# Performance work log

Hardware: AMD Instinct MI355X
Metric: run time of the kernel (lower is better)

Reference implementation:

```python
import math
import jax, jax.numpy as jnp
import numpy as np

B, L, D = 16, 2048, 64  # batch, seq len (m == n, self-attention), head dim
C = 30                   # ProbSparse sampling factor c


def setup_inputs() -> dict:
    key = jax.random.key(0)
    kq, kk, kv = jax.random.split(key, 3)
    Q = jax.random.normal(kq, (B, L, D), dtype=jnp.float32)
    K = jax.random.normal(kk, (B, L, D), dtype=jnp.float32)
    V = jax.random.normal(kv, (B, L, D), dtype=jnp.float32)
    return {"Q": Q, "K": K, "V": V, "seed": 0}


def reference(Q, K, V, seed):
    b, m, d = Q.shape
    n = K.shape[1]
    u = int(C * math.log(m))              # number of active queries
    U = min(int(m * math.log(n)), n)      # number of sampled keys (clamped to n)
    inv_sqrt_d = 1.0 / math.sqrt(d)

    rngs = jax.random.split(jax.random.key(seed), b)

    def _each_sample(Qb, Kb, Vb, r):
        # random sample of U key rows without replacement
        idx = jax.random.choice(r, n, shape=(U,), replace=False)
        Kbar = Kb[idx]                                # [U, d]
        Sbar = jnp.matmul(Qb, Kbar.T)                 # [m, U]
        M = jnp.max(Sbar, axis=1) - jnp.mean(Sbar, axis=1)  # sparsity measure [m]
        _, I = jax.lax.top_k(M, u)                    # active query indices [u]
        Qbar = Qb[I]                                  # [u, d]
        A = jax.nn.softmax(jnp.matmul(Qbar, Kb.T) * inv_sqrt_d, axis=-1)  # [u, n]
        S1 = jnp.matmul(A, Vb)                        # [u, d]
        # literal source: fill with mean(V, axis=1, keepdims=True) -> (n,1) broadcast (m==n)
        S = jnp.broadcast_to(jnp.mean(Vb, axis=1, keepdims=True), (m, d))
        return S.at[I].set(S1)

    return jax.vmap(_each_sample)(Q, K, V, rngs)
```

## Files before the change

### kernel.cpp

```cpp
#include <hip/hip_runtime.h>

#define NB 16
#define NN 2048
#define DH 64
#define NSEL 228
#define KS 8
#define CHUNK (NN / KS)
#define RS 8

__global__ __launch_bounds__(256, 2) void rowstat_kernel(const float* __restrict__ Q,
                                                         const float* __restrict__ K,
                                                         float* __restrict__ Mmax,
                                                         float* __restrict__ Msum) {
  __shared__ float Qt[32][128];
  __shared__ float Kt[32][128];
  const int b = blockIdx.y;
  const int cz = blockIdx.z;
  const int qbase = blockIdx.x * 128;
  const int tid = threadIdx.x;
  const int r = tid & 127;
  const int h16 = (tid >> 7) * 16;
  const int ty = tid >> 4;
  const int tx = tid & 15;
  const float* Qb = Q + ((size_t)b * NN + qbase) * DH;
  const float* Kb = K + ((size_t)b * NN + cz * (NN / RS)) * DH;

  float rmax[8], rsum[8];
  #pragma unroll
  for (int a = 0; a < 8; ++a) { rmax[a] = -3.0e38f; rsum[a] = 0.f; }

  for (int kt = 0; kt < NN / RS / 128; ++kt) {
    float acc[8][8];
    #pragma unroll
    for (int a = 0; a < 8; ++a)
      #pragma unroll
      for (int c = 0; c < 8; ++c) acc[a][c] = 0.f;

    #pragma unroll
    for (int half = 0; half < 2; ++half) {
      const int d0 = half * 32;
      __syncthreads();
      {
        const float* qs = Qb + r * DH + d0 + h16;
        const float* ks = Kb + ((size_t)(kt * 128 + r)) * DH + d0 + h16;
        #pragma unroll
        for (int f = 0; f < 4; ++f) {
          float4 v = *reinterpret_cast<const float4*>(qs + f * 4);
          Qt[h16 + f * 4 + 0][r] = v.x;
          Qt[h16 + f * 4 + 1][r] = v.y;
          Qt[h16 + f * 4 + 2][r] = v.z;
          Qt[h16 + f * 4 + 3][r] = v.w;
          float4 w = *reinterpret_cast<const float4*>(ks + f * 4);
          Kt[h16 + f * 4 + 0][r] = w.x;
          Kt[h16 + f * 4 + 1][r] = w.y;
          Kt[h16 + f * 4 + 2][r] = w.z;
          Kt[h16 + f * 4 + 3][r] = w.w;
        }
      }
      __syncthreads();

      #pragma unroll 2
      for (int d = 0; d < 32; ++d) {
        float qv[8], kv[8];
        *reinterpret_cast<float4*>(qv) =
            *reinterpret_cast<const float4*>(&Qt[d][ty * 4]);
        *reinterpret_cast<float4*>(qv + 4) =
            *reinterpret_cast<const float4*>(&Qt[d][64 + ty * 4]);
        *reinterpret_cast<float4*>(kv) =
            *reinterpret_cast<const float4*>(&Kt[d][tx * 4]);
        *reinterpret_cast<float4*>(kv + 4) =
            *reinterpret_cast<const float4*>(&Kt[d][64 + tx * 4]);
        #pragma unroll
        for (int a = 0; a < 8; ++a)
          #pragma unroll
          for (int c = 0; c < 8; ++c) acc[a][c] = fmaf(qv[a], kv[c], acc[a][c]);
      }
    }

    #pragma unroll
    for (int a = 0; a < 8; ++a)
      #pragma unroll
      for (int c = 0; c < 8; ++c) {
        rmax[a] = fmaxf(rmax[a], acc[a][c]);
        rsum[a] += acc[a][c];
      }
  }

  #pragma unroll
  for (int off = 1; off < 16; off <<= 1) {
    #pragma unroll
    for (int a = 0; a < 8; ++a) {
      rmax[a] = fmaxf(rmax[a], __shfl_xor(rmax[a], off));
      rsum[a] += __shfl_xor(rsum[a], off);
    }
  }
  if (tx == 0) {
    #pragma unroll
    for (int a = 0; a < 8; ++a) {
      const int qlocal = (a >> 2) * 64 + ty * 4 + (a & 3);
      const size_t idx = ((size_t)cz * NB + b) * NN + qbase + qlocal;
      Mmax[idx] = rmax[a];
      Msum[idx] = rsum[a];
    }
  }
}

__global__ __launch_bounds__(256) void select_kernel(const float* __restrict__ Mmax,
                                                     const float* __restrict__ Msum,
                                                     int* __restrict__ Isel) {
  __shared__ int red[4];
  const int b = blockIdx.x;
  const int tid = threadIdx.x;
  const int lane = tid & 63;
  const int wid = tid >> 6;
  const int base = tid * 8;

  unsigned int kreg[8];
  #pragma unroll
  for (int f = 0; f < 8; ++f) {
    const int i = base + f;
    float mv = -3.0e38f, sv = 0.f;
    #pragma unroll
    for (int cz = 0; cz < RS; ++cz) {
      const size_t idx = ((size_t)cz * NB + b) * NN + i;
      mv = fmaxf(mv, Mmax[idx]);
      sv += Msum[idx];
    }
    const float M = mv - sv * (1.0f / NN);
    const unsigned int uu = __float_as_uint(M);
    kreg[f] = (uu & 0x80000000u) ? ~uu : (uu | 0x80000000u);
  }

  unsigned int v = 0u;
  for (int bit = 31; bit >= 0; --bit) {
    const unsigned int cand = v | (1u << bit);
    int c = 0;
    #pragma unroll
    for (int f = 0; f < 8; ++f) c += (kreg[f] >= cand) ? 1 : 0;
    #pragma unroll
    for (int off = 1; off < 64; off <<= 1) c += __shfl_xor(c, off);
    if (lane == 0) red[wid] = c;
    __syncthreads();
    const int total = red[0] + red[1] + red[2] + red[3];
    if (total >= NSEL) v = cand;
    __syncthreads();
  }

  int flg[8];
  int cnt = 0;
  #pragma unroll
  for (int f = 0; f < 8; ++f) { flg[f] = (kreg[f] > v) ? 1 : 0; cnt += flg[f]; }
  int scan = cnt;
  #pragma unroll
  for (int off = 1; off < 64; off <<= 1) {
    const int n = __shfl_up(scan, off);
    if (lane >= off) scan += n;
  }
  if (lane == 63) red[wid] = scan;
  __syncthreads();
  int wbase = 0;
  for (int w = 0; w < wid; ++w) wbase += red[w];
  const int cg = red[0] + red[1] + red[2] + red[3];
  int pos = wbase + scan - cnt;
  #pragma unroll
  for (int f = 0; f < 8; ++f)
    if (flg[f]) { Isel[b * NSEL + pos] = base + f; ++pos; }
  __syncthreads();

  const int need = NSEL - cg;
  cnt = 0;
  #pragma unroll
  for (int f = 0; f < 8; ++f) { flg[f] = (kreg[f] == v) ? 1 : 0; cnt += flg[f]; }
  scan = cnt;
  #pragma unroll
  for (int off = 1; off < 64; off <<= 1) {
    const int n = __shfl_up(scan, off);
    if (lane >= off) scan += n;
  }
  if (lane == 63) red[wid] = scan;
  __syncthreads();
  wbase = 0;
  for (int w = 0; w < wid; ++w) wbase += red[w];
  pos = wbase + scan - cnt;
  #pragma unroll
  for (int f = 0; f < 8; ++f)
    if (flg[f]) {
      if (pos < need) Isel[b * NSEL + cg + pos] = base + f;
      ++pos;
    }
}

__global__ __launch_bounds__(256) void fill_kernel(const float* __restrict__ V,
                                                   float* __restrict__ out) {
  const size_t row = (size_t)blockIdx.x * 4 + (threadIdx.x >> 6);
  const int lane = threadIdx.x & 63;
  float x = V[row * DH + lane];
  #pragma unroll
  for (int off = 1; off < 64; off <<= 1) x += __shfl_xor(x, off);
  out[row * DH + lane] = x * (1.0f / DH);
}

__global__ __launch_bounds__(256) void attn_part_kernel(const float* __restrict__ Q,
                                                        const float* __restrict__ K,
                                                        const float* __restrict__ V,
                                                        const int* __restrict__ Isel,
                                                        float* __restrict__ Pm,
                                                        float* __restrict__ Pl,
                                                        float* __restrict__ Po) {
  __shared__ float Qt[64][32];
  __shared__ float Kt[64][64];
  __shared__ float Vs[64][64];
  __shared__ float Pt[64][36];
  const int b = blockIdx.z;
  const int kc = blockIdx.y;
  const int g = blockIdx.x;
  const int tid = threadIdx.x;
  const int wq = tid >> 5;
  const int kx = tid & 31;

  if (tid < 128) {
    const int rr = tid >> 2;
    const int dblk = (tid & 3) * 16;
    const int lq = g * 32 + rr;
    const int qidx = (lq < NSEL) ? Isel[b * NSEL + lq] : 0;
    const float* qs = Q + ((size_t)b * NN + qidx) * DH + dblk;
    #pragma unroll
    for (int f = 0; f < 4; ++f) {
      float4 v = *reinterpret_cast<const float4*>(qs + f * 4);
      Qt[dblk + f * 4 + 0][rr] = v.x;
      Qt[dblk + f * 4 + 1][rr] = v.y;
      Qt[dblk + f * 4 + 2][rr] = v.z;
      Qt[dblk + f * 4 + 3][rr] = v.w;
    }
  }

  const float* Kb = K + ((size_t)b * NN + kc * CHUNK) * DH;
  const float* Vb = V + ((size_t)b * NN + kc * CHUNK) * DH;

  float m[4], lp[4], o[4][2];
  #pragma unroll
  for (int a = 0; a < 4; ++a) {
    m[a] = -3.0e38f; lp[a] = 0.f; o[a][0] = 0.f; o[a][1] = 0.f;
  }

  for (int st = 0; st < CHUNK / 64; ++st) {
    __syncthreads();
    {
      const int rr = tid & 63;
      const int dblk = (tid >> 6) * 16;
      const float* ks = Kb + ((size_t)(st * 64 + rr)) * DH + dblk;
      #pragma unroll
      for (int f = 0; f < 4; ++f) {
        float4 v = *reinterpret_cast<const float4*>(ks + f * 4);
        Kt[dblk + f * 4 + 0][rr] = v.x;
        Kt[dblk + f * 4 + 1][rr] = v.y;
        Kt[dblk + f * 4 + 2][rr] = v.z;
        Kt[dblk + f * 4 + 3][rr] = v.w;
      }
      const float* vsrc = Vb + (size_t)st * 64 * DH;
      float* vdst = &Vs[0][0];
      #pragma unroll
      for (int it = 0; it < 4; ++it) {
        const int fo = (it * 256 + tid) * 4;
        *reinterpret_cast<float4*>(vdst + fo) =
            *reinterpret_cast<const float4*>(vsrc + fo);
      }
    }
    __syncthreads();

    float sc[4][2];
    #pragma unroll
    for (int a = 0; a < 4; ++a) { sc[a][0] = 0.f; sc[a][1] = 0.f; }
    #pragma unroll 4
    for (int d = 0; d < 64; ++d) {
      float qv[4];
      *reinterpret_cast<float4*>(qv) =
          *reinterpret_cast<const float4*>(&Qt[d][wq * 4]);
      const float2 kv = *reinterpret_cast<const float2*>(&Kt[d][kx * 2]);
      #pragma unroll
      for (int a = 0; a < 4; ++a) {
        sc[a][0] = fmaf(qv[a], kv.x, sc[a][0]);
        sc[a][1] = fmaf(qv[a], kv.y, sc[a][1]);
      }
    }
    #pragma unroll
    for (int a = 0; a < 4; ++a) { sc[a][0] *= 0.125f; sc[a][1] *= 0.125f; }

    float tm[4];
    #pragma unroll
    for (int a = 0; a < 4; ++a) tm[a] = fmaxf(sc[a][0], sc[a][1]);
    #pragma unroll
    for (int off = 1; off < 32; off <<= 1) {
      #pragma unroll
      for (int a = 0; a < 4; ++a) tm[a] = fmaxf(tm[a], __shfl_xor(tm[a], off));
    }

    float w0[4], w1[4];
    #pragma unroll
    for (int a = 0; a < 4; ++a) {
      const float mn = fmaxf(m[a], tm[a]);
      const float scale = __expf(m[a] - mn);
      m[a] = mn;
      lp[a] *= scale;
      o[a][0] *= scale;
      o[a][1] *= scale;
      w0[a] = __expf(sc[a][0] - mn);
      w1[a] = __expf(sc[a][1] - mn);
      lp[a] += w0[a] + w1[a];
    }
    *reinterpret_cast<float4*>(&Pt[kx * 2][wq * 4]) =
        make_float4(w0[0], w0[1], w0[2], w0[3]);
    *reinterpret_cast<float4*>(&Pt[kx * 2 + 1][wq * 4]) =
        make_float4(w1[0], w1[1], w1[2], w1[3]);
    __syncthreads();

    #pragma unroll 4
    for (int k = 0; k < 64; ++k) {
      float pv[4];
      *reinterpret_cast<float4*>(pv) =
          *reinterpret_cast<const float4*>(&Pt[k][wq * 4]);
      const float2 vv = *reinterpret_cast<const float2*>(&Vs[k][kx * 2]);
      #pragma unroll
      for (int a = 0; a < 4; ++a) {
        o[a][0] = fmaf(pv[a], vv.x, o[a][0]);
        o[a][1] = fmaf(pv[a], vv.y, o[a][1]);
      }
    }
  }

  #pragma unroll
  for (int off = 1; off < 32; off <<= 1) {
    #pragma unroll
    for (int a = 0; a < 4; ++a) lp[a] += __shfl_xor(lp[a], off);
  }

  #pragma unroll
  for (int a = 0; a < 4; ++a) {
    const int lq = g * 32 + wq * 4 + a;
    if (lq < NSEL) {
      const size_t row = ((size_t)b * NSEL + lq) * KS + kc;
      if (kx == 0) { Pm[row] = m[a]; Pl[row] = lp[a]; }
      *reinterpret_cast<float2*>(Po + row * 64 + kx * 2) =
          make_float2(o[a][0], o[a][1]);
    }
  }
}

__global__ __launch_bounds__(256) void combine_kernel(const int* __restrict__ Isel,
                                                      const float* __restrict__ Pm,
                                                      const float* __restrict__ Pl,
                                                      const float* __restrict__ Po,
                                                      float* __restrict__ out) {
  const int r = blockIdx.x * 4 + (threadIdx.x >> 6);
  if (r >= NB * NSEL) return;
  const int lane = threadIdx.x & 63;
  const int b = r / NSEL;
  const int qidx = Isel[r];
  const size_t base = (size_t)r * KS;

  float pm[KS];
  float gm = -3.0e38f;
  #pragma unroll
  for (int c = 0; c < KS; ++c) { pm[c] = Pm[base + c]; gm = fmaxf(gm, pm[c]); }
  float L = 0.f, od = 0.f;
  #pragma unroll
  for (int c = 0; c < KS; ++c) {
    const float e = __expf(pm[c] - gm);
    L += Pl[base + c] * e;
    od += Po[(base + c) * 64 + lane] * e;
  }
  out[((size_t)b * NN + qidx) * DH + lane] = od / L;
}

extern "C" void kernel_launch(void* const* d_in, const int* in_sizes, int n_in,
                              void* d_out, int out_size, void* d_ws, size_t ws_size,
                              hipStream_t stream) {
  const float* Q = (const float*)d_in[0];
  const float* K = (const float*)d_in[1];
  const float* V = (const float*)d_in[2];
  float* out = (float*)d_out;

  float* Mmax = (float*)d_ws;
  float* Msum = Mmax + (size_t)RS * NB * NN;
  int* Isel = (int*)(Msum + (size_t)RS * NB * NN);
  float* Pm = (float*)(Isel + NB * NSEL);
  float* Pl = Pm + (size_t)NB * NSEL * KS;
  float* Po = Pl + (size_t)NB * NSEL * KS;

  rowstat_kernel<<<dim3(NN / 128, NB, RS), 256, 0, stream>>>(Q, K, Mmax, Msum);
  select_kernel<<<dim3(NB), 256, 0, stream>>>(Mmax, Msum, Isel);
  fill_kernel<<<dim3(NB * NN / 4), 256, 0, stream>>>(V, out);
  attn_part_kernel<<<dim3(8, KS, NB), 256, 0, stream>>>(Q, K, V, Isel, Pm, Pl, Po);
  combine_kernel<<<dim3((NB * NSEL + 3) / 4), 256, 0, stream>>>(Isel, Pm, Pl, Po, out);
}
```

Before: 254.4 us.

## Compute row max via split-bf16 MFMA and row mean via key column sums

Replaces the fp32 FMA row-statistics GEMM with a bf16 hi/lo split MFMA kernel (three products) and drops the per-row sum. Each row mean is now computed algebraically as Q·colsum(K)/N from a small column-sum kernel. Rows whose sparsity score falls within an epsilon band of the top-k threshold get an exact fp32 max recomputation before the final selection. This trades the full fp32 GEMM for tensor-core work plus conversion kernels, and relies on the epsilon band being wide enough to keep the selection exact.

```diff
diff --git a/kernel.cpp b/kernel.cpp
--- a/kernel.cpp
+++ b/kernel.cpp
@@ -6,131 +6,151 @@
 #define NSEL 228
 #define KS 8
 #define CHUNK (NN / KS)
-#define RS 8
-
-__global__ __launch_bounds__(256, 2) void rowstat_kernel(const float* __restrict__ Q,
-                                                         const float* __restrict__ K,
-                                                         float* __restrict__ Mmax,
-                                                         float* __restrict__ Msum) {
-  __shared__ float Qt[32][128];
-  __shared__ float Kt[32][128];
-  const int b = blockIdx.y;
-  const int cz = blockIdx.z;
+#define RS 4
+#define EPSBAND 2.0e-3f
+
+using s16x8 = __attribute__((ext_vector_type(8))) short;
+using f32x16 = __attribute__((ext_vector_type(16))) float;
+
+static __device__ __forceinline__ unsigned short f2bf(float x) {
+  unsigned int u = __float_as_uint(x);
+  u += 0x7fffu + ((u >> 16) & 1u);
+  return (unsigned short)(u >> 16);
+}
+static __device__ __forceinline__ float bf2f(unsigned short h) {
+  return __uint_as_float(((unsigned int)h) << 16);
+}
+static __device__ __forceinline__ unsigned int enc(float f) {
+  unsigned int u = __float_as_uint(f);
+  return (u & 0x80000000u) ? ~u : (u | 0x80000000u);
+}
+static __device__ __forceinline__ float dec(unsigned int k) {
+  return (k & 0x80000000u) ? __uint_as_float(k & 0x7fffffffu)
+                           : __uint_as_float(~k);
+}
+
+__global__ __launch_bounds__(256) void convk_kernel(const float* __restrict__ K,
+                                                    unsigned short* __restrict__ Khi,
+                                                    unsigned short* __restrict__ Klo) {
+  const size_t e = ((size_t)blockIdx.x * 256 + threadIdx.x) * 8;
+  float4 a = *(const float4*)(K + e);
+  float4 b = *(const float4*)(K + e + 4);
+  float v[8] = {a.x, a.y, a.z, a.w, b.x, b.y, b.z, b.w};
+  union { unsigned short u[8]; s16x8 s; } H, L;
+  #pragma unroll
+  for (int j = 0; j < 8; ++j) {
+    unsigned short h = f2bf(v[j]);
+    H.u[j] = h;
+    L.u[j] = f2bf(v[j] - bf2f(h));
+  }
+  *(s16x8*)(Khi + e) = H.s;
+  *(s16x8*)(Klo + e) = L.s;
+}
+
+__global__ __launch_bounds__(256) void kcolsum_kernel(const float* __restrict__ K,
+                                                      float* __restrict__ Kpart) {
+  __shared__ float part[4][64];
+  const int b = blockIdx.y, ch = blockIdx.x;
+  const int d = threadIdx.x & 63, g = threadIdx.x >> 6;
+  const float* Kb = K + ((size_t)b * NN + ch * 128) * DH;
+  float s = 0.f;
+  for (int r = g; r < 128; r += 4) s += Kb[r * DH + d];
+  part[g][d] = s;
+  __syncthreads();
+  if (threadIdx.x < 64)
+    Kpart[((size_t)b * 16 + ch) * 64 + threadIdx.x] =
+        part[0][threadIdx.x] + part[1][threadIdx.x] +
+        part[2][threadIdx.x] + part[3][threadIdx.x];
+}
+
+__global__ __launch_bounds__(256, 4) void rowstat_mfma(const float* __restrict__ Q,
+                                                       const unsigned short* __restrict__ Khi,
+                                                       const unsigned short* __restrict__ Klo,
+                                                       float* __restrict__ Mmax) {
+  __shared__ __align__(16) unsigned short KHs[128 * 64];
+  __shared__ __align__(16) unsigned short KLs[128 * 64];
+  const int b = blockIdx.y, cz = blockIdx.z;
   const int qbase = blockIdx.x * 128;
   const int tid = threadIdx.x;
-  const int r = tid & 127;
-  const int h16 = (tid >> 7) * 16;
-  const int ty = tid >> 4;
-  const int tx = tid & 15;
-  const float* Qb = Q + ((size_t)b * NN + qbase) * DH;
-  const float* Kb = K + ((size_t)b * NN + cz * (NN / RS)) * DH;
-
-  float rmax[8], rsum[8];
-  #pragma unroll
-  for (int a = 0; a < 8; ++a) { rmax[a] = -3.0e38f; rsum[a] = 0.f; }
-
-  for (int kt = 0; kt < NN / RS / 128; ++kt) {
-    float acc[8][8];
-    #pragma unroll
-    for (int a = 0; a < 8; ++a)
-      #pragma unroll
-      for (int c = 0; c < 8; ++c) acc[a][c] = 0.f;
-
-    #pragma unroll
-    for (int half = 0; half < 2; ++half) {
-      const int d0 = half * 32;
-      __syncthreads();
-      {
-        const float* qs = Qb + r * DH + d0 + h16;
-        const float* ks = Kb + ((size_t)(kt * 128 + r)) * DH + d0 + h16;
-        #pragma unroll
-        for (int f = 0; f < 4; ++f) {
-          float4 v = *reinterpret_cast<const float4*>(qs + f * 4);
-          Qt[h16 + f * 4 + 0][r] = v.x;
-          Qt[h16 + f * 4 + 1][r] = v.y;
-          Qt[h16 + f * 4 + 2][r] = v.z;
-          Qt[h16 + f * 4 + 3][r] = v.w;
-          float4 w = *reinterpret_cast<const float4*>(ks + f * 4);
-          Kt[h16 + f * 4 + 0][r] = w.x;
-          Kt[h16 + f * 4 + 1][r] = w.y;
-          Kt[h16 + f * 4 + 2][r] = w.z;
-          Kt[h16 + f * 4 + 3][r] = w.w;
-        }
-      }
-      __syncthreads();
-
-      #pragma unroll 2
-      for (int d = 0; d < 32; ++d) {
-        float qv[8], kv[8];
-        *reinterpret_cast<float4*>(qv) =
-            *reinterpret_cast<const float4*>(&Qt[d][ty * 4]);
-        *reinterpret_cast<float4*>(qv + 4) =
-            *reinterpret_cast<const float4*>(&Qt[d][64 + ty * 4]);
-        *reinterpret_cast<float4*>(kv) =
-            *reinterpret_cast<const float4*>(&Kt[d][tx * 4]);
-        *reinterpret_cast<float4*>(kv + 4) =
-            *reinterpret_cast<const float4*>(&Kt[d][64 + tx * 4]);
-        #pragma unroll
-        for (int a = 0; a < 8; ++a)
-          #pragma unroll
-          for (int c = 0; c < 8; ++c) acc[a][c] = fmaf(qv[a], kv[c], acc[a][c]);
-      }
-    }
-
-    #pragma unroll
-    for (int a = 0; a < 8; ++a)
-      #pragma unroll
-      for (int c = 0; c < 8; ++c) {
-        rmax[a] = fmaxf(rmax[a], acc[a][c]);
-        rsum[a] += acc[a][c];
-      }
-  }
-
-  #pragma unroll
-  for (int off = 1; off < 16; off <<= 1) {
-    #pragma unroll
-    for (int a = 0; a < 8; ++a) {
-      rmax[a] = fmaxf(rmax[a], __shfl_xor(rmax[a], off));
-      rsum[a] += __shfl_xor(rsum[a], off);
-    }
-  }
-  if (tx == 0) {
-    #pragma unroll
-    for (int a = 0; a < 8; ++a) {
-      const int qlocal = (a >> 2) * 64 + ty * 4 + (a & 3);
-      const size_t idx = ((size_t)cz * NB + b) * NN + qbase + qlocal;
-      Mmax[idx] = rmax[a];
-      Msum[idx] = rsum[a];
-    }
-  }
-}
-
-__global__ __launch_bounds__(256) void select_kernel(const float* __restrict__ Mmax,
-                                                     const float* __restrict__ Msum,
-                                                     int* __restrict__ Isel) {
-  __shared__ int red[4];
-  const int b = blockIdx.x;
-  const int tid = threadIdx.x;
-  const int lane = tid & 63;
-  const int wid = tid >> 6;
-  const int base = tid * 8;
-
-  unsigned int kreg[8];
-  #pragma unroll
-  for (int f = 0; f < 8; ++f) {
-    const int i = base + f;
-    float mv = -3.0e38f, sv = 0.f;
-    #pragma unroll
-    for (int cz = 0; cz < RS; ++cz) {
-      const size_t idx = ((size_t)cz * NB + b) * NN + i;
-      mv = fmaxf(mv, Mmax[idx]);
-      sv += Msum[idx];
-    }
-    const float M = mv - sv * (1.0f / NN);
-    const unsigned int uu = __float_as_uint(M);
-    kreg[f] = (uu & 0x80000000u) ? ~uu : (uu | 0x80000000u);
-  }
-
+  const int w = tid >> 6, lane = tid & 63;
+  const int l31 = lane & 31, hi5 = lane >> 5;
+
+  s16x8 qh[4], ql[4];
+  {
+    const float* qrow = Q + ((size_t)b * NN + qbase + w * 32 + l31) * DH;
+    #pragma unroll
+    for (int ks = 0; ks < 4; ++ks) {
+      const int d0 = ks * 16 + hi5 * 8;
+      float4 x = *(const float4*)(qrow + d0);
+      float4 y = *(const float4*)(qrow + d0 + 4);
+      float v[8] = {x.x, x.y, x.z, x.w, y.x, y.y, y.z, y.w};
+      union { unsigned short u[8]; s16x8 s; } H, L;
+      #pragma unroll
+      for (int j = 0; j < 8; ++j) {
+        unsigned short h = f2bf(v[j]);
+        H.u[j] = h;
+        L.u[j] = f2bf(v[j] - bf2f(h));
+      }
+      qh[ks] = H.s;
+      ql[ks] = L.s;
+    }
+  }
+
+  const size_t kbase = ((size_t)b * NN + cz * (NN / RS)) * DH;
+  f32x16 vmax;
+  #pragma unroll
+  for (int i = 0; i < 16; ++i) vmax[i] = -3.0e38f;
+
+  const int sr = tid >> 1;
+  const int sh = tid & 1;
+
+  for (int stage = 0; stage < NN / RS / 128; ++stage) {
+    __syncthreads();
+    {
+      const size_t g = kbase + (size_t)(stage * 128 + sr) * DH + sh * 32;
+      const unsigned short* gh = Khi + g;
+      const unsigned short* gl = Klo + g;
+      #pragma unroll
+      for (int c = 0; c < 4; ++c) {
+        s16x8 hv = *(const s16x8*)(gh + c * 8);
+        s16x8 lv = *(const s16x8*)(gl + c * 8);
+        const int chn = (sh * 4 + c) ^ (sr & 7);
+        *(s16x8*)&KHs[(sr * 8 + chn) * 8] = hv;
+        *(s16x8*)&KLs[(sr * 8 + chn) * 8] = lv;
+      }
+    }
+    __syncthreads();
+
+    #pragma unroll
+    for (int ksub = 0; ksub < 4; ++ksub) {
+      const int kr = ksub * 32 + l31;
+      f32x16 acc;
+      #pragma unroll
+      for (int i = 0; i < 16; ++i) acc[i] = 0.f;
+      #pragma unroll
+      for (int ks = 0; ks < 4; ++ks) {
+        const int chn = (ks * 2 + hi5) ^ (kr & 7);
+        s16x8 ah = *(const s16x8*)&KHs[(kr * 8 + chn) * 8];
+        s16x8 al = *(const s16x8*)&KLs[(kr * 8 + chn) * 8];
+        acc = __builtin_amdgcn_mfma_f32_32x32x16_bf16(ah, qh[ks], acc, 0, 0, 0);
+        acc = __builtin_amdgcn_mfma_f32_32x32x16_bf16(al, qh[ks], acc, 0, 0, 0);
+        acc = __builtin_amdgcn_mfma_f32_32x32x16_bf16(ah, ql[ks], acc, 0, 0, 0);
+      }
+      #pragma unroll
+      for (int i = 0; i < 16; ++i) vmax[i] = fmaxf(vmax[i], acc[i]);
+    }
+  }
+
+  float m = vmax[0];
+  #pragma unroll
+  for (int i = 1; i < 16; ++i) m = fmaxf(m, vmax[i]);
+  m = fmaxf(m, __shfl_xor(m, 32));
+  if (lane < 32)
+    Mmax[((size_t)cz * NB + b) * NN + qbase + w * 32 + lane] = m;
+}
+
+static __device__ unsigned int radix_thresh(const unsigned int* kreg, int lane,
+                                            int wid, int* red) {
   unsigned int v = 0u;
   for (int bit = 31; bit >= 0; --bit) {
     const unsigned int cand = v | (1u << bit);
@@ -141,25 +161,123 @@
     for (int off = 1; off < 64; off <<= 1) c += __shfl_xor(c, off);
     if (lane == 0) red[wid] = c;
     __syncthreads();
-    const int total = red[0] + red[1] + red[2] + red[3];
-    if (total >= NSEL) v = cand;
-    __syncthreads();
-  }
+    if (red[0] + red[1] + red[2] + red[3] >= NSEL) v = cand;
+    __syncthreads();
+  }
+  return v;
+}
+
+__global__ __launch_bounds__(256) void select_kernel(const float* __restrict__ Q,
+                                                     const float* __restrict__ K,
+                                                     const float* __restrict__ Mmax,
+                                                     const float* __restrict__ Kpart,
+                                                     int* __restrict__ Isel) {
+  __shared__ unsigned int keys[NN];
+  __shared__ float meanv[NN];
+  __shared__ int list_[NN];
+  __shared__ float qsh[64];
+  __shared__ float Ksl[64];
+  __shared__ float fred[4];
+  __shared__ int red[4];
+  __shared__ int cntS;
+  const int b = blockIdx.x;
+  const int tid = threadIdx.x;
+  const int lane = tid & 63, wid = tid >> 6;
+  const int base = tid * 8;
+
+  if (tid < 64) {
+    float s = 0.f;
+    for (int c = 0; c < 16; ++c) s += Kpart[((size_t)b * 16 + c) * 64 + tid];
+    Ksl[tid] = s;
+  }
+  if (tid == 0) cntS = 0;
+  __syncthreads();
+
+  for (int f = 0; f < 8; ++f) {
+    const int i = base + f;
+    float mv = -3.0e38f;
+    #pragma unroll
+    for (int cz = 0; cz < RS; ++cz)
+      mv = fmaxf(mv, Mmax[((size_t)cz * NB + b) * NN + i]);
+    const float* qrow = Q + ((size_t)b * NN + i) * DH;
+    float s = 0.f;
+    #pragma unroll
+    for (int d4 = 0; d4 < 16; ++d4) {
+      float4 qv = *(const float4*)(qrow + d4 * 4);
+      s = fmaf(qv.x, Ksl[d4 * 4 + 0], s);
+      s = fmaf(qv.y, Ksl[d4 * 4 + 1], s);
+      s = fmaf(qv.z, Ksl[d4 * 4 + 2], s);
+      s = fmaf(qv.w, Ksl[d4 * 4 + 3], s);
+    }
+    const float mean = s * (1.0f / NN);
+    meanv[i] = mean;
+    keys[i] = enc(mv - mean);
+  }
+  __syncthreads();
+
+  unsigned int kreg[8];
+  #pragma unroll
+  for (int f = 0; f < 8; ++f) kreg[f] = keys[base + f];
+
+  const unsigned int v1 = radix_thresh(kreg, lane, wid, red);
+  const float vf = dec(v1);
+
+  #pragma unroll
+  for (int f = 0; f < 8; ++f) {
+    if (fabsf(dec(kreg[f]) - vf) <= EPSBAND) {
+      int p = atomicAdd(&cntS, 1);
+      list_[p] = base + f;
+    }
+  }
+  __syncthreads();
+  const int nband = cntS;
+  for (int n = 0; n < nband; ++n) {
+    const int row = list_[n];
+    if (tid < 64) qsh[tid] = Q[((size_t)b * NN + row) * DH + tid];
+    __syncthreads();
+    float lmax = -3.0e38f;
+    for (int j = tid; j < NN; j += 256) {
+      const float* krow = K + ((size_t)b * NN + j) * DH;
+      float s = 0.f;
+      #pragma unroll
+      for (int d4 = 0; d4 < 16; ++d4) {
+        float4 kv = *(const float4*)(krow + d4 * 4);
+        s = fmaf(kv.x, qsh[d4 * 4 + 0], s);
+        s = fmaf(kv.y, qsh[d4 * 4 + 1], s);
+        s = fmaf(kv.z, qsh[d4 * 4 + 2], s);
+        s = fmaf(kv.w, qsh[d4 * 4 + 3], s);
+      }
+      lmax = fmaxf(lmax, s);
+    }
+    #pragma unroll
+    for (int off = 1; off < 64; off <<= 1) lmax = fmaxf(lmax, __shfl_xor(lmax, off));
+    if (lane == 0) fred[wid] = lmax;
+    __syncthreads();
+    if (tid == 0) {
+      const float mx = fmaxf(fmaxf(fred[0], fred[1]), fmaxf(fred[2], fred[3]));
+      keys[row] = enc(mx - meanv[row]);
+    }
+    __syncthreads();
+  }
+  #pragma unroll
+  for (int f = 0; f < 8; ++f) kreg[f] = keys[base + f];
+
+  const unsigned int v2 = radix_thresh(kreg, lane, wid, red);
 
   int flg[8];
   int cnt = 0;
   #pragma unroll
-  for (int f = 0; f < 8; ++f) { flg[f] = (kreg[f] > v) ? 1 : 0; cnt += flg[f]; }
+  for (int f = 0; f < 8; ++f) { flg[f] = (kreg[f] > v2) ? 1 : 0; cnt += flg[f]; }
   int scan = cnt;
   #pragma unroll
   for (int off = 1; off < 64; off <<= 1) {
-    const int n = __shfl_up(scan, off);
-    if (lane >= off) scan += n;
+    const int t = __shfl_up(scan, off);
+    if (lane >= off) scan += t;
   }
   if (lane == 63) red[wid] = scan;
   __syncthreads();
   int wbase = 0;
-  for (int w = 0; w < wid; ++w) wbase += red[w];
+  for (int ww = 0; ww < wid; ++ww) wbase += red[ww];
   const int cg = red[0] + red[1] + red[2] + red[3];
   int pos = wbase + scan - cnt;
   #pragma unroll
@@ -170,17 +288,17 @@
   const int need = NSEL - cg;
   cnt = 0;
   #pragma unroll
-  for (int f = 0; f < 8; ++f) { flg[f] = (kreg[f] == v) ? 1 : 0; cnt += flg[f]; }
+  for (int f = 0; f < 8; ++f) { flg[f] = (kreg[f] == v2) ? 1 : 0; cnt += flg[f]; }
   scan = cnt;
   #pragma unroll
   for (int off = 1; off < 64; off <<= 1) {
-    const int n = __shfl_up(scan, off);
-    if (lane >= off) scan += n;
+    const int t = __shfl_up(scan, off);
+    if (lane >= off) scan += t;
   }
   if (lane == 63) red[wid] = scan;
   __syncthreads();
   wbase = 0;
-  for (int w = 0; w < wid; ++w) wbase += red[w];
+  for (int ww = 0; ww < wid; ++ww) wbase += red[ww];
   pos = wbase + scan - cnt;
   #pragma unroll
   for (int f = 0; f < 8; ++f)
@@ -381,14 +499,18 @@
   float* out = (float*)d_out;
 
   float* Mmax = (float*)d_ws;
-  float* Msum = Mmax + (size_t)RS * NB * NN;
-  int* Isel = (int*)(Msum + (size_t)RS * NB * NN);
+  float* Kpart = Mmax + (size_t)RS * NB * NN;
+  int* Isel = (int*)(Kpart + (size_t)NB * 16 * 64);
   float* Pm = (float*)(Isel + NB * NSEL);
   float* Pl = Pm + (size_t)NB * NSEL * KS;
   float* Po = Pl + (size_t)NB * NSEL * KS;
-
-  rowstat_kernel<<<dim3(NN / 128, NB, RS), 256, 0, stream>>>(Q, K, Mmax, Msum);
-  select_kernel<<<dim3(NB), 256, 0, stream>>>(Mmax, Msum, Isel);
+  unsigned short* Khi = (unsigned short*)(Po + (size_t)NB * NSEL * KS * 64);
+  unsigned short* Klo = Khi + (size_t)NB * NN * DH;
+
+  convk_kernel<<<dim3((NB * NN * DH) / (256 * 8)), 256, 0, stream>>>(K, Khi, Klo);
+  kcolsum_kernel<<<dim3(16, NB), 256, 0, stream>>>(K, Kpart);
+  rowstat_mfma<<<dim3(NN / 128, NB, RS), 256, 0, stream>>>(Q, Khi, Klo, Mmax);
+  select_kernel<<<dim3(NB), 256, 0, stream>>>(Q, K, Mmax, Kpart, Isel);
   fill_kernel<<<dim3(NB * NN / 4), 256, 0, stream>>>(V, out);
   attn_part_kernel<<<dim3(8, KS, NB), 256, 0, stream>>>(Q, K, V, Isel, Pm, Pl, Po);
   combine_kernel<<<dim3((NB * NSEL + 3) / 4), 256, 0, stream>>>(Isel, Pm, Pl, Po, out);
```

New measurement: 242.0 us. -4.8%, faster.
